# Performance work log

Hardware: AMD Instinct MI355X
Metric: run time of the kernel (lower is better)

The kernel has to match this reference:

```python
import jax, jax.numpy as jnp
import numpy as np

EMB_DIM = 1024
HEAD_SIZE = 64
B, T = 4, 4096


def setup_inputs() -> dict:
    key = jax.random.key(0)
    kx, kq, kk, kv = jax.random.split(key, 4)
    scale = 1.0 / np.sqrt(EMB_DIM)
    x = jax.random.normal(kx, (B, T, EMB_DIM), dtype=jnp.float32)
    # weights stored as [emb_dim, head_size] so projection is x @ W
    Wq = jax.random.normal(kq, (EMB_DIM, HEAD_SIZE), dtype=jnp.float32) * scale
    Wk = jax.random.normal(kk, (EMB_DIM, HEAD_SIZE), dtype=jnp.float32) * scale
    Wv = jax.random.normal(kv, (EMB_DIM, HEAD_SIZE), dtype=jnp.float32) * scale
    return {"x": x, "Wq": Wq, "Wk": Wk, "Wv": Wv}


def reference(x, Wq, Wk, Wv):
    # Single causal self-attention head. NOTE: original scales by emb_dim**-0.5
    # (d = x.shape[-1]), not head_size**-0.5 — we reproduce that faithfully.
    _, t, d = x.shape
    q = jnp.einsum('bte,eh->bth', x, Wq)
    k = jnp.einsum('bte,eh->bth', x, Wk)
    v = jnp.einsum('bte,eh->bth', x, Wv)
    wei = jnp.einsum('bth,bsh->bts', q, k) * (d ** -0.5)  # [B, T, T]
    causal = jnp.tril(jnp.ones((t, t), dtype=bool))
    wei = jnp.where(causal, wei, -jnp.inf)
    attn = jax.nn.softmax(wei, axis=-1)
    out = jnp.einsum('bts,bsh->bth', attn, v)  # [B, T, head_size]
    return out
```

## Files before the change

kernel.cpp:

```cpp
#include <hip/hip_runtime.h>
#include <hip/hip_bf16.h>

#define EMB   1024
#define HS    64
#define BATCH 4
#define SEQ   4096
#define MTOT  (BATCH*SEQ)

typedef float  f32x4 __attribute__((ext_vector_type(4)));
typedef short  s16x8 __attribute__((ext_vector_type(8)));
typedef __bf16 bf16x8 __attribute__((ext_vector_type(8)));

__device__ __forceinline__ unsigned short f2bf(float f) {
    unsigned int u = __float_as_uint(f);
    u = (u + 0x7fffu + ((u >> 16) & 1u)) >> 16;
    return (unsigned short)u;
}
__device__ __forceinline__ unsigned int pkbf(float lo, float hi) {
#if __has_builtin(__builtin_amdgcn_cvt_pk_bf16_f32)
    return __builtin_bit_cast(unsigned int,
        __builtin_amdgcn_cvt_pk_bf16_f32(lo, hi));
#else
    return (unsigned int)f2bf(lo) | ((unsigned int)f2bf(hi) << 16);
#endif
}
__device__ __forceinline__ s16x8 cvt8(float4 a, float4 b) {
    union { unsigned int u[4]; s16x8 v; } r;
    r.u[0] = pkbf(a.x, a.y); r.u[1] = pkbf(a.z, a.w);
    r.u[2] = pkbf(b.x, b.y); r.u[3] = pkbf(b.z, b.w);
    return r.v;
}
__device__ __forceinline__ f32x4 mfma16(s16x8 a, s16x8 b, f32x4 c) {
    return __builtin_amdgcn_mfma_f32_16x16x32_bf16(
        __builtin_bit_cast(bf16x8, a), __builtin_bit_cast(bf16x8, b), c, 0, 0, 0);
}
__device__ __forceinline__ void ld_lds16(const unsigned short* g, unsigned short* l) {
    __builtin_amdgcn_global_load_lds(
        (const __attribute__((address_space(1))) unsigned int*)g,
        (__attribute__((address_space(3))) unsigned int*)l, 16, 0, 0);
}

__global__ __launch_bounds__(256) void pack_w(const float* __restrict__ Wq,
                                              const float* __restrict__ Wk,
                                              const float* __restrict__ Wv,
                                              unsigned short* __restrict__ wp) {
    int idx = blockIdx.x * 256 + threadIdx.x;
    int l = idx & 63;
    int s = (idx >> 6) & 31;
    int t = idx >> 11;
    const float* W = (t < 4) ? Wq : (t < 8) ? Wk : Wv;
    float scale = (t < 4) ? 0.03125f : 1.0f;
    int n  = ((t & 3) * 16) + (l & 15);
    int k0 = s * 32 + ((l >> 4) * 8);
    s16x8 v;
#pragma unroll
    for (int j = 0; j < 8; j++)
        v[j] = (short)f2bf(W[(size_t)(k0 + j) * HS + n] * scale);
    *(s16x8*)(wp + (size_t)idx * 8) = v;
}

__global__ __launch_bounds__(256) void proj(const float* __restrict__ x,
                                            const unsigned short* __restrict__ wp,
                                            unsigned short* __restrict__ qws,
                                            unsigned short* __restrict__ kws,
                                            unsigned short* __restrict__ vtws) {
    __shared__ unsigned short vt[16][72];
    int l = threadIdx.x & 63, w = threadIdx.x >> 6;
    int lane15 = l & 15, quad = l >> 4;
    int row0 = blockIdx.x * 16;

    const float* xp = x + (size_t)(row0 + lane15) * EMB + quad * 8;
    const unsigned short* wb0 = wp + (size_t)l * 8;

    s16x8 wb[2][3];
    float4 xb[2][2];
#pragma unroll
    for (int p = 0; p < 2; p++) {
#pragma unroll
        for (int j = 0; j < 3; j++)
            wb[p][j] = *(const s16x8*)(wb0 + (size_t)((w + 4 * j) * 32 + p) * 512);
        xb[p][0] = *(const float4*)(xp + p * 32);
        xb[p][1] = *(const float4*)(xp + p * 32 + 4);
    }

    f32x4 acc[3] = {};
#pragma unroll 2
    for (int s = 0; s < 32; s++) {
        int cur = s & 1;
        s16x8 af = cvt8(xb[cur][0], xb[cur][1]);
#pragma unroll
        for (int j = 0; j < 3; j++)
            acc[j] = mfma16(af, wb[cur][j], acc[j]);
        if (s < 30) {
#pragma unroll
            for (int j = 0; j < 3; j++)
                wb[cur][j] = *(const s16x8*)(
                    wb0 + (size_t)((w + 4 * j) * 32 + s + 2) * 512);
            xb[cur][0] = *(const float4*)(xp + (s + 2) * 32);
            xb[cur][1] = *(const float4*)(xp + (s + 2) * 32 + 4);
        }
    }

#pragma unroll
    for (int r = 0; r < 4; r++) {
        int row = row0 + quad * 4 + r;
        qws[(size_t)row * HS + w * 16 + lane15] = f2bf(acc[0][r]);
        kws[(size_t)row * HS + w * 16 + lane15] = f2bf(acc[1][r]);
        vt[quad * 4 + r][w * 16 + lane15] = f2bf(acc[2][r]);
    }
    __syncthreads();
    if (threadIdx.x < 64) {
        int h = threadIdx.x;
        int b = row0 >> 12, tp0 = row0 & (SEQ - 1);
        unsigned short tmp[16];
#pragma unroll
        for (int j = 0; j < 16; j++) tmp[j] = vt[j][h];
        unsigned short* dst = vtws + ((size_t)b * HS + h) * SEQ + tp0;
        *(s16x8*)dst       = *(s16x8*)tmp;
        *(s16x8*)(dst + 8) = *(s16x8*)(tmp + 8);
    }
}

__global__ __launch_bounds__(256) void attn_part(const unsigned short* __restrict__ qws,
                                                 const unsigned short* __restrict__ kws,
                                                 const unsigned short* __restrict__ vtws,
                                                 float* __restrict__ op,
                                                 float* __restrict__ lp) {
    __shared__ unsigned short ldsK[2][4096];
    __shared__ unsigned short ldsV[2][4096];
    __shared__ unsigned short plds[4][16][72];

    int l = threadIdx.x & 63;
    int w = threadIdx.x >> 6;
    int lane15 = l & 15, quad = l >> 4;

    int W = blockIdx.x;
    int b = W / 288;
    int g = W - b * 288;
    int n = 1;
    while (g >= 4 * n * (n + 1)) n++;
    int off = g - 4 * n * (n - 1);
    int oQ  = (unsigned)off / (unsigned)n;
    int Q   = 8 * (n - 1) + oQ;
    int c   = off - oQ * n;
    int lenT = Q + 1;
    int t0 = c * 8;
    int t1 = min(t0 + 8, lenT);
    int q0 = Q * 64 + w * 16;
    int diag = lenT - 1;

    auto stage = [&](int buf, int c0) {
#pragma unroll
        for (int j = 0; j < 2; j++) {
            int s = w + j * 4;
            int t = s >> 1, h = s & 1;
            ld_lds16(kws + ((size_t)b * SEQ + c0 + t * 16 + lane15) * HS
                         + h * 32 + quad * 8,
                     &ldsK[buf][s * 512]);
            ld_lds16(vtws + ((size_t)b * HS + t * 16 + lane15) * SEQ
                          + c0 + h * 32 + quad * 8,
                     &ldsV[buf][s * 512]);
        }
    };

    const unsigned short* qbase =
        qws + ((size_t)b * SEQ + q0 + lane15) * HS + quad * 8;
    s16x8 qf0 = *(const s16x8*)(qbase);
    s16x8 qf1 = *(const s16x8*)(qbase + 32);

    f32x4 o[4] = {};
    float lsum[4] = {0.f, 0.f, 0.f, 0.f};

    stage(0, t0 * 64);
    int buf = 0;
    for (int kt = t0; kt < t1; kt++) {
        __syncthreads();
        if (kt + 1 < t1) stage(buf ^ 1, (kt + 1) * 64);

        f32x4 sacc[4] = {};
#pragma unroll
        for (int t = 0; t < 4; t++) {
            s16x8 kf0 = *(const s16x8*)(&ldsK[buf][(2 * t) * 512 + l * 8]);
            s16x8 kf1 = *(const s16x8*)(&ldsK[buf][(2 * t + 1) * 512 + l * 8]);
            sacc[t] = mfma16(qf0, kf0, sacc[t]);
            sacc[t] = mfma16(qf1, kf1, sacc[t]);
        }

        if (kt == diag) {
            int c0 = kt * 64;
#pragma unroll
            for (int t = 0; t < 4; t++)
#pragma unroll
                for (int r = 0; r < 4; r++) {
                    int qrow = q0 + quad * 4 + r;
                    int kcol = c0 + t * 16 + lane15;
                    if (kcol > qrow) sacc[t][r] = -1e30f;
                }
        }

#pragma unroll
        for (int t = 0; t < 4; t++)
#pragma unroll
            for (int r = 0; r < 4; r++) {
                float p = __expf(sacc[t][r]);
                lsum[r] += p;
                plds[w][quad * 4 + r][t * 16 + lane15] = f2bf(p);
            }
        __builtin_amdgcn_s_waitcnt(0xC07F);

#pragma unroll
        for (int c2 = 0; c2 < 2; c2++) {
            s16x8 pf = *(const s16x8*)(&plds[w][lane15][c2 * 32 + quad * 8]);
#pragma unroll
            for (int t = 0; t < 4; t++) {
                s16x8 vf = *(const s16x8*)(&ldsV[buf][(2 * t + c2) * 512 + l * 8]);
                o[t] = mfma16(pf, vf, o[t]);
            }
        }
        buf ^= 1;
    }

#pragma unroll
    for (int r = 0; r < 4; r++) {
#pragma unroll
        for (int d = 1; d < 16; d <<= 1)
            lsum[r] += __shfl_xor(lsum[r], d, 64);
    }

    size_t slot = (size_t)b * 288 + g;
    float* ob = op + slot * 4096;
#pragma unroll
    for (int t = 0; t < 4; t++)
#pragma unroll
        for (int r = 0; r < 4; r++)
            ob[(w * 16 + quad * 4 + r) * 64 + t * 16 + lane15] = o[t][r];
    if (lane15 == 0) {
#pragma unroll
        for (int r = 0; r < 4; r++)
            lp[slot * 64 + w * 16 + quad * 4 + r] = lsum[r];
    }
}

__global__ __launch_bounds__(256) void attn_combine(const float* __restrict__ op,
                                                    const float* __restrict__ lp,
                                                    float* __restrict__ out) {
    int e = blockIdx.x * 256 + threadIdx.x;
    int c4 = (e & 15) * 4;
    int row = e >> 4;
    int b   = row >> 12;
    int tr  = row & (SEQ - 1);
    int Q   = tr >> 6;
    int r64 = tr & 63;
    int n   = (Q >> 3) + 1;
    int g0  = 4 * n * (n - 1) + (Q - 8 * (n - 1)) * n;
    f32x4 os = {0.f, 0.f, 0.f, 0.f};
    float ls = 0.f;
    for (int c = 0; c < n; c++) {
        size_t slot = (size_t)b * 288 + g0 + c;
        os += *(const f32x4*)(op + slot * 4096 + r64 * 64 + c4);
        ls += lp[slot * 64 + r64];
    }
    f32x4 r = os / ls;
    *(f32x4*)(out + (size_t)row * HS + c4) = r;
}

extern "C" void kernel_launch(void* const* d_in, const int* in_sizes, int n_in,
                              void* d_out, int out_size, void* d_ws, size_t ws_size,
                              hipStream_t stream) {
    const float* x  = (const float*)d_in[0];
    const float* Wq = (const float*)d_in[1];
    const float* Wk = (const float*)d_in[2];
    const float* Wv = (const float*)d_in[3];
    float* out = (float*)d_out;

    unsigned short* ws   = (unsigned short*)d_ws;
    unsigned short* wp   = ws;
    unsigned short* qws  = ws + 262144;
    unsigned short* kws  = ws + 1310720;
    unsigned short* vtws = ws + 2359296;
    float* op = (float*)(ws + 3407872);
    float* lp = op + 4718592;

    hipLaunchKernelGGL(pack_w,      dim3(96),   dim3(256), 0, stream, Wq, Wk, Wv, wp);
    hipLaunchKernelGGL(proj,        dim3(1024), dim3(256), 0, stream, x, wp, qws, kws, vtws);
    hipLaunchKernelGGL(attn_part,   dim3(1152), dim3(256), 0, stream, qws, kws, vtws, op, lp);
    hipLaunchKernelGGL(attn_combine,dim3(1024), dim3(256), 0, stream, op, lp, out);
}
```

Before: 171.3 us.

## Stage projection x and weights through LDS with async loads and 32-row tiles

The projection kernel now processes 32 rows per block instead of 16. It stages x and the packed weight tiles into double-buffered LDS using global_load_lds, with an XOR swizzle on the x tile. Each wave computes 6 MFMA outputs, reusing each weight fragment across two row halves, which halves redundant weight reads and cuts register-held prefetch buffers. The cost is a __syncthreads per k-step, and the grid shrinks to 512 blocks, which lowers parallelism.

After: 158.6 us. 1.08x faster.

```diff
diff --git a/kernel.cpp b/kernel.cpp
--- a/kernel.cpp
+++ b/kernel.cpp
@@ -34,7 +34,7 @@
     return __builtin_amdgcn_mfma_f32_16x16x32_bf16(
         __builtin_bit_cast(bf16x8, a), __builtin_bit_cast(bf16x8, b), c, 0, 0, 0);
 }
-__device__ __forceinline__ void ld_lds16(const unsigned short* g, unsigned short* l) {
+__device__ __forceinline__ void ld_lds16(const void* g, unsigned short* l) {
     __builtin_amdgcn_global_load_lds(
         (const __attribute__((address_space(1))) unsigned int*)g,
         (__attribute__((address_space(3))) unsigned int*)l, 16, 0, 0);
@@ -64,58 +64,71 @@
                                             unsigned short* __restrict__ qws,
                                             unsigned short* __restrict__ kws,
                                             unsigned short* __restrict__ vtws) {
-    __shared__ unsigned short vt[16][72];
+    __shared__ unsigned short xb[2][2048];
+    __shared__ unsigned short wb[2][6144];
+    __shared__ unsigned short vt[32][72];
     int l = threadIdx.x & 63, w = threadIdx.x >> 6;
     int lane15 = l & 15, quad = l >> 4;
-    int row0 = blockIdx.x * 16;
-
-    const float* xp = x + (size_t)(row0 + lane15) * EMB + quad * 8;
-    const unsigned short* wb0 = wp + (size_t)l * 8;
-
-    s16x8 wb[2][3];
-    float4 xb[2][2];
-#pragma unroll
-    for (int p = 0; p < 2; p++) {
-#pragma unroll
-        for (int j = 0; j < 3; j++)
-            wb[p][j] = *(const s16x8*)(wb0 + (size_t)((w + 4 * j) * 32 + p) * 512);
-        xb[p][0] = *(const float4*)(xp + p * 32);
-        xb[p][1] = *(const float4*)(xp + p * 32 + 4);
-    }
-
-    f32x4 acc[3] = {};
-#pragma unroll 2
-    for (int s = 0; s < 32; s++) {
-        int cur = s & 1;
-        s16x8 af = cvt8(xb[cur][0], xb[cur][1]);
-#pragma unroll
-        for (int j = 0; j < 3; j++)
-            acc[j] = mfma16(af, wb[cur][j], acc[j]);
-        if (s < 30) {
-#pragma unroll
-            for (int j = 0; j < 3; j++)
-                wb[cur][j] = *(const s16x8*)(
-                    wb0 + (size_t)((w + 4 * j) * 32 + s + 2) * 512);
-            xb[cur][0] = *(const float4*)(xp + (s + 2) * 32);
-            xb[cur][1] = *(const float4*)(xp + (s + 2) * 32 + 4);
-        }
+    int rh = w & 1, ts = w >> 1;
+    int row0 = blockIdx.x * 32;
+
+    auto stage = [&](int buf, int sg) {
+        int d = w * 64 + l;
+        int row = d >> 3, cs = d & 7;
+        int sc = cs ^ (row & 7);
+        ld_lds16(x + (size_t)(row0 + row) * EMB + sg * 32 + sc * 4,
+                 &xb[buf][w * 512]);
+#pragma unroll
+        for (int j = 0; j < 3; j++) {
+            int f = w + 4 * j;
+            ld_lds16(wp + ((size_t)(f * 32 + sg) * 64 + l) * 8,
+                     &wb[buf][f * 512]);
+        }
+    };
+
+    int xrow = rh * 16 + lane15;
+    int rsw = xrow & 7;
+    f32x4 acc[6] = {};
+
+    stage(0, 0);
+    int buf = 0;
+    for (int sg = 0; sg < 32; sg++) {
+        __syncthreads();
+        if (sg < 31) stage(buf ^ 1, sg + 1);
+
+        float4 lo = *(const float4*)&xb[buf][(xrow * 8 + ((2 * quad)     ^ rsw)) * 8];
+        float4 hi = *(const float4*)&xb[buf][(xrow * 8 + ((2 * quad + 1) ^ rsw)) * 8];
+        s16x8 af = cvt8(lo, hi);
+#pragma unroll
+        for (int j = 0; j < 6; j++) {
+            int t = ts + 2 * j;
+            s16x8 bfr = *(const s16x8*)&wb[buf][t * 512 + l * 8];
+            acc[j] = mfma16(af, bfr, acc[j]);
+        }
+        buf ^= 1;
     }
 
 #pragma unroll
     for (int r = 0; r < 4; r++) {
-        int row = row0 + quad * 4 + r;
-        qws[(size_t)row * HS + w * 16 + lane15] = f2bf(acc[0][r]);
-        kws[(size_t)row * HS + w * 16 + lane15] = f2bf(acc[1][r]);
-        vt[quad * 4 + r][w * 16 + lane15] = f2bf(acc[2][r]);
+        int row = row0 + rh * 16 + quad * 4 + r;
+#pragma unroll
+        for (int j = 0; j < 2; j++) {
+            int tq = ts + 2 * j;
+            int tk = ts + 2 * j + 4;
+            int tv = ts + 2 * j + 8;
+            qws[(size_t)row * HS + tq * 16 + lane15] = f2bf(acc[j][r]);
+            kws[(size_t)row * HS + (tk - 4) * 16 + lane15] = f2bf(acc[j + 2][r]);
+            vt[rh * 16 + quad * 4 + r][(tv - 8) * 16 + lane15] = f2bf(acc[j + 4][r]);
+        }
     }
     __syncthreads();
-    if (threadIdx.x < 64) {
-        int h = threadIdx.x;
+    if (threadIdx.x < 128) {
+        int h = threadIdx.x & 63, half = threadIdx.x >> 6;
         int b = row0 >> 12, tp0 = row0 & (SEQ - 1);
         unsigned short tmp[16];
 #pragma unroll
-        for (int j = 0; j < 16; j++) tmp[j] = vt[j][h];
-        unsigned short* dst = vtws + ((size_t)b * HS + h) * SEQ + tp0;
+        for (int j = 0; j < 16; j++) tmp[j] = vt[half * 16 + j][h];
+        unsigned short* dst = vtws + ((size_t)b * HS + h) * SEQ + tp0 + half * 16;
         *(s16x8*)dst       = *(s16x8*)tmp;
         *(s16x8*)(dst + 8) = *(s16x8*)(tmp + 8);
     }
@@ -282,7 +295,7 @@
     float* lp = op + 4718592;
 
     hipLaunchKernelGGL(pack_w,      dim3(96),   dim3(256), 0, stream, Wq, Wk, Wv, wp);
-    hipLaunchKernelGGL(proj,        dim3(1024), dim3(256), 0, stream, x, wp, qws, kws, vtws);
+    hipLaunchKernelGGL(proj,        dim3(512),  dim3(256), 0, stream, x, wp, qws, kws, vtws);
     hipLaunchKernelGGL(attn_part,   dim3(1152), dim3(256), 0, stream, qws, kws, vtws, op, lp);
     hipLaunchKernelGGL(attn_combine,dim3(1024), dim3(256), 0, stream, op, lp, out);
 }
```
